# Kernel tuning notes

Hardware: AMD Instinct MI355X
Metric: run time of the kernel (lower is better)

Reference implementation:

```python
import jax, jax.numpy as jnp
from jax import lax
import numpy as np

D_IN, D_H, M_BANK = 1024, 512, 100


def setup_inputs() -> dict:
    key = jax.random.key(0)
    ks = jax.random.split(key, 12)
    B, T = 128, 256
    s = 0.01
    return {
        "hidden_frames": jax.random.normal(ks[0], (B, T, D_IN), jnp.float32),
        # hidden_to_content: Linear(hidden+input -> hidden)
        "W_c": jax.random.normal(ks[1], (D_H + D_IN, D_H), jnp.float32) * s,
        "b_c": jnp.zeros((D_H,), jnp.float32),
        # read_prob: Linear(hidden+input -> memory_bank_size)
        "W_rp": jax.random.normal(ks[2], (D_H + D_IN, M_BANK), jnp.float32) * s,
        "b_rp": jnp.zeros((M_BANK,), jnp.float32),
        # write_prob: Linear(hidden+input -> memory_bank_size)
        "W_wp": jax.random.normal(ks[3], (D_H + D_IN, M_BANK), jnp.float32) * s,
        "b_wp": jnp.zeros((M_BANK,), jnp.float32),
        # RNN cell params (init: normal(0, 0.01), bias zero)
        "Wxh": jax.random.normal(ks[4], (D_IN, D_H), jnp.float32) * s,
        "Wrh": jax.random.normal(ks[5], (D_H, D_H), jnp.float32) * s,
        "Whh": jax.random.normal(ks[6], (D_H, D_H), jnp.float32) * s,
        "bh": jnp.zeros((D_H,), jnp.float32),
        "nImg": 256,
    }


def reference(hidden_frames, W_c, b_c, W_rp, b_rp, W_wp, b_wp, Wxh, Wrh, Whh, bh, nImg):
    B = hidden_frames.shape[0]
    H = Wxh.shape[1]
    M = W_rp.shape[1]

    def step(carry, x_t):
        # x_t: (B, D_in); h: (B, H); mem: (B, M, H)
        h, mem = carry
        xh = jnp.concatenate([x_t, h], axis=-1)            # (B, D_in+H)
        ar = jax.nn.softmax(xh @ W_rp + b_rp, axis=-1)     # (B, M) read weights
        r = jnp.einsum('bm,bmh->bh', ar, mem)              # (B, H) read vector
        h_new = jax.nn.relu(x_t @ Wxh + r @ Wrh + h @ Whh + bh)
        c = jax.nn.relu(xh @ W_c + b_c)                    # (B, H) write content
        aw = jax.nn.softmax(xh @ W_wp + b_wp, axis=-1)[:, :, None]  # (B, M, 1)
        mem = aw * c[:, None, :] + (1.0 - aw) * mem        # gated blend overwrite
        return (h_new, mem), h_new

    xs = jnp.swapaxes(hidden_frames[:, :nImg, :], 0, 1)    # (T, B, D_in)
    h0 = jnp.zeros((B, H), hidden_frames.dtype)
    mem0 = jnp.zeros((B, M, H), hidden_frames.dtype)
    _, hs = lax.scan(step, (h0, mem0), xs)                 # hs: (T, B, H)
    return jnp.swapaxes(hs, 0, 1)                          # (B, T, H)
```

## Files before the change

kernel.cpp:

```cpp
#include <hip/hip_runtime.h>

#define D_IN   1024
#define D_H    512
#define M_BANK 100
#define BATCH  128
#define NCOL   1224
#define NPAD   1280
#define KTOT   1536
#define KSH    4

typedef unsigned short u16;
typedef __attribute__((ext_vector_type(8))) short s16x8;
typedef __attribute__((ext_vector_type(4))) float f32x4;

__device__ __forceinline__ u16 f2bf(float f) {
  union { float f; unsigned int u; } v;
  v.f = f;
  unsigned int r = (v.u + 0x7FFFu + ((v.u >> 16) & 1u)) >> 16;
  return (u16)r;
}
__device__ __forceinline__ float bf2f(u16 b) {
  union { unsigned int u; float f; } v;
  v.u = ((unsigned int)b) << 16;
  return v.f;
}

__global__ void k_prep_w(const float* __restrict__ W_c,
                         const float* __restrict__ W_rp,
                         const float* __restrict__ W_wp,
                         const float* __restrict__ Wxh,
                         const float* __restrict__ Whh,
                         u16* __restrict__ W_bt) {
  const int j = blockIdx.x;
  const int k = blockIdx.y * 256 + threadIdx.x;
  float v = 0.f;
  if (j < 100)       v = W_rp[(size_t)k * M_BANK + j];
  else if (j < 200)  v = W_wp[(size_t)k * M_BANK + (j - 100)];
  else if (j < 712)  v = W_c[(size_t)k * D_H + (j - 200)];
  else if (j < NCOL) v = (k < D_IN) ? Wxh[(size_t)k * D_H + (j - 712)]
                                    : Whh[(size_t)(k - D_IN) * D_H + (j - 712)];
  W_bt[(size_t)j * KTOT + k] = f2bf(v);
}

__global__ void k_prep_wrh(const float* __restrict__ Wrh,
                           u16* __restrict__ Wrh_bf) {
  const int i = blockIdx.x * 256 + threadIdx.x;
  Wrh_bf[i] = f2bf(Wrh[i]);
}

__global__ void k_zx_mfma(const float* __restrict__ frames,
                          const u16* __restrict__ W_bt,
                          float* __restrict__ zx,
                          int t0, int CH, int lgCH, int TF) {
  __shared__ u16 Asb[64][40];
  __shared__ u16 Bsb[64][40];
  const int tid  = threadIdx.x;
  const int lane = tid & 63;
  const int wid  = tid >> 6;
  const int wm   = wid >> 1, wn = wid & 1;
  const int j0 = blockIdx.x * 64;
  const int r0 = blockIdx.y * 64;
  const int srow = tid >> 2;
  const int skk  = (tid & 3) * 8;
  const int gr = r0 + srow;
  const int b  = gr >> lgCH;
  const int tc = gr & (CH - 1);
  const float* arow = &frames[((size_t)b * TF + t0 + tc) * D_IN];
  const u16*   brow = &W_bt[(size_t)(j0 + srow) * KTOT];

  f32x4 a00 = {0.f, 0.f, 0.f, 0.f}, a01 = {0.f, 0.f, 0.f, 0.f};
  f32x4 a10 = {0.f, 0.f, 0.f, 0.f}, a11 = {0.f, 0.f, 0.f, 0.f};

  for (int k0 = 0; k0 < D_IN; k0 += 32) {
    const float4 v0 = *reinterpret_cast<const float4*>(&arow[k0 + skk]);
    const float4 v1 = *reinterpret_cast<const float4*>(&arow[k0 + skk + 4]);
    s16x8 a8;
    a8[0] = (short)f2bf(v0.x); a8[1] = (short)f2bf(v0.y);
    a8[2] = (short)f2bf(v0.z); a8[3] = (short)f2bf(v0.w);
    a8[4] = (short)f2bf(v1.x); a8[5] = (short)f2bf(v1.y);
    a8[6] = (short)f2bf(v1.z); a8[7] = (short)f2bf(v1.w);
    *reinterpret_cast<s16x8*>(&Asb[srow][skk]) = a8;
    *reinterpret_cast<s16x8*>(&Bsb[srow][skk]) =
        *reinterpret_cast<const s16x8*>(&brow[k0 + skk]);
    __syncthreads();
    const int ka = (lane >> 4) * 8;
    const s16x8 af0 = *reinterpret_cast<s16x8*>(&Asb[wm * 32 + (lane & 15)][ka]);
    const s16x8 af1 = *reinterpret_cast<s16x8*>(&Asb[wm * 32 + 16 + (lane & 15)][ka]);
    const s16x8 bf0 = *reinterpret_cast<s16x8*>(&Bsb[wn * 32 + (lane & 15)][ka]);
    const s16x8 bf1 = *reinterpret_cast<s16x8*>(&Bsb[wn * 32 + 16 + (lane & 15)][ka]);
    a00 = __builtin_amdgcn_mfma_f32_16x16x32_bf16(af0, bf0, a00, 0, 0, 0);
    a01 = __builtin_amdgcn_mfma_f32_16x16x32_bf16(af0, bf1, a01, 0, 0, 0);
    a10 = __builtin_amdgcn_mfma_f32_16x16x32_bf16(af1, bf0, a10, 0, 0, 0);
    a11 = __builtin_amdgcn_mfma_f32_16x16x32_bf16(af1, bf1, a11, 0, 0, 0);
    __syncthreads();
  }
  const int rb = r0 + wm * 32 + (lane >> 4) * 4;
  const int cb = j0 + wn * 32 + (lane & 15);
#define STORE_ACC(A, MF, NF)                                             \
  {                                                                      \
    _Pragma("unroll")                                                    \
    for (int reg = 0; reg < 4; ++reg)                                    \
      zx[(size_t)(rb + MF * 16 + reg) * NPAD + cb + NF * 16] = A[reg];   \
  }
  STORE_ACC(a00, 0, 0) STORE_ACC(a01, 0, 1) STORE_ACC(a10, 1, 0) STORE_ACC(a11, 1, 1)
#undef STORE_ACC
}

__global__ void __launch_bounds__(256)
k_zh_mfma(const u16* __restrict__ h_bf,
          const u16* __restrict__ W_bt,
          float* __restrict__ zhp) {
  __shared__ u16 Asb[64][136];
  __shared__ u16 Bsb[64][136];
  const int tid  = threadIdx.x;
  const int lane = tid & 63;
  const int wid  = tid >> 6;
  const int wm   = wid >> 1, wn = wid & 1;
  const int j0 = blockIdx.x * 64;
  const int r0 = blockIdx.y * 64;
  const int kp = blockIdx.z;
  const int srow = tid >> 2;
  const int sseg = (tid & 3) * 32;
  const u16* arow = &h_bf[(size_t)(r0 + srow) * D_H + kp * 128 + sseg];
  const u16* brow = &W_bt[(size_t)(j0 + srow) * KTOT + D_IN + kp * 128 + sseg];

  #pragma unroll
  for (int i = 0; i < 4; ++i) {
    *reinterpret_cast<s16x8*>(&Asb[srow][sseg + i * 8]) =
        *reinterpret_cast<const s16x8*>(&arow[i * 8]);
    *reinterpret_cast<s16x8*>(&Bsb[srow][sseg + i * 8]) =
        *reinterpret_cast<const s16x8*>(&brow[i * 8]);
  }
  __syncthreads();

  f32x4 a00 = {0.f, 0.f, 0.f, 0.f}, a01 = {0.f, 0.f, 0.f, 0.f};
  f32x4 a10 = {0.f, 0.f, 0.f, 0.f}, a11 = {0.f, 0.f, 0.f, 0.f};
  const int la = lane & 15;
  #pragma unroll
  for (int kk = 0; kk < 4; ++kk) {
    const int ka = kk * 32 + (lane >> 4) * 8;
    const s16x8 af0 = *reinterpret_cast<s16x8*>(&Asb[wm * 32 + la][ka]);
    const s16x8 af1 = *reinterpret_cast<s16x8*>(&Asb[wm * 32 + 16 + la][ka]);
    const s16x8 bf0 = *reinterpret_cast<s16x8*>(&Bsb[wn * 32 + la][ka]);
    const s16x8 bf1 = *reinterpret_cast<s16x8*>(&Bsb[wn * 32 + 16 + la][ka]);
    a00 = __builtin_amdgcn_mfma_f32_16x16x32_bf16(af0, bf0, a00, 0, 0, 0);
    a01 = __builtin_amdgcn_mfma_f32_16x16x32_bf16(af0, bf1, a01, 0, 0, 0);
    a10 = __builtin_amdgcn_mfma_f32_16x16x32_bf16(af1, bf0, a10, 0, 0, 0);
    a11 = __builtin_amdgcn_mfma_f32_16x16x32_bf16(af1, bf1, a11, 0, 0, 0);
  }
  const int rb = r0 + wm * 32 + (lane >> 4) * 4;
  const int cb = j0 + wn * 32 + (lane & 15);
  float* zp = &zhp[(size_t)kp * BATCH * NPAD];
#define STORE_ACC(A, MF, NF)                                             \
  {                                                                      \
    _Pragma("unroll")                                                    \
    for (int reg = 0; reg < 4; ++reg)                                    \
      zp[(size_t)(rb + MF * 16 + reg) * NPAD + cb + NF * 16] = A[reg];   \
  }
  STORE_ACC(a00, 0, 0) STORE_ACC(a01, 0, 1) STORE_ACC(a10, 1, 0) STORE_ACC(a11, 1, 1)
#undef STORE_ACC
}

__global__ void __launch_bounds__(512)
k_phase2(const float* __restrict__ zx,
         const float* __restrict__ zhp,
         const u16* __restrict__ Wrh_bf,
         const float* __restrict__ b_rp,
         const float* __restrict__ b_wp,
         const float* __restrict__ b_c,
         const float* __restrict__ bh,
         u16* __restrict__ M2b,
         float* __restrict__ out,
         u16* __restrict__ h_bf,
         int t, int tc, int CH, int T) {
  __shared__ float ar_s[2][M_BANK];
  __shared__ float aw_s[2][M_BANK];
  __shared__ float c_s[2][D_H];
  __shared__ float red[2][16][32][4];
  __shared__ float smx[2][2][2];
  __shared__ float ssm[2][2][2];
  const int tid  = threadIdx.x;
  const int ba   = tid >> 8;
  const int lane = tid & 31;
  const int p    = blockIdx.x;
  const int b0   = blockIdx.y * 2;
  const int b_g  = b0 + ba;
  const int s0   = p * 128 + lane * 4;
  const bool hz  = (t > 0);
  const size_t zxrow = (size_t)(b_g * CH + tc) * NPAD;

  {
    const int u     = tid & 255;
    const int which = u >> 7;
    const int m     = u & 127;
    const int wv    = (u >> 6) & 1;
    float l = -1e30f;
    if (m < M_BANK) {
      const int col = which * 100 + m;
      l = (which ? b_wp[m] : b_rp[m]) + zx[zxrow + col];
      if (hz) {
        #pragma unroll
        for (int q = 0; q < KSH; ++q)
          l += zhp[(size_t)(q * BATCH + b_g) * NPAD + col];
      }
    }
    float mx = l;
    #pragma unroll
    for (int o = 32; o; o >>= 1) mx = fmaxf(mx, __shfl_xor(mx, o, 64));
    if ((tid & 63) == 0) smx[ba][which][wv] = mx;
    __syncthreads();
    mx = fmaxf(smx[ba][which][0], smx[ba][which][1]);
    const float e = (m < M_BANK) ? __expf(l - mx) : 0.f;
    float s = e;
    #pragma unroll
    for (int o = 32; o; o >>= 1) s += __shfl_xor(s, o, 64);
    if ((tid & 63) == 0) ssm[ba][which][wv] = s;
    __syncthreads();
    s = ssm[ba][which][0] + ssm[ba][which][1];
    if (m < M_BANK) {
      const float a = e / s;
      if (which) aw_s[ba][m] = a;
      else       ar_s[ba][m] = a;
    }
  }
  for (int idx = tid; idx < 2 * D_H; idx += 512) {
    const int bb  = idx >> 9;
    const int k   = idx & 511;
    const int bg2 = b0 + bb;
    float v = b_c[k] + zx[(size_t)(bg2 * CH + tc) * NPAD + 200 + k];
    if (hz) {
      #pragma unroll
      for (int q = 0; q < KSH; ++q)
        v += zhp[(size_t)(q * BATCH + bg2) * NPAD + 200 + k];
    }
    c_s[bb][k] = fmaxf(v, 0.f);
  }
  __syncthreads();

  {
    const int g = tid >> 5;
    float cwa[4] = {};
    float cwb[4] = {};
    const int kbase = g * 32;
    #pragma unroll 8
    for (int kk = 0; kk < 32; ++kk) {
      const int k = kbase + kk;
      const ushort4 w4 = *reinterpret_cast<const ushort4*>(&Wrh_bf[(size_t)k * D_H + s0]);
      const float w0 = bf2f(w4.x), w1 = bf2f(w4.y), w2 = bf2f(w4.z), w3 = bf2f(w4.w);
      const float ca = c_s[0][k];
      const float cb = c_s[1][k];
      cwa[0] += ca * w0; cwa[1] += ca * w1; cwa[2] += ca * w2; cwa[3] += ca * w3;
      cwb[0] += cb * w0; cwb[1] += cb * w1; cwb[2] += cb * w2; cwb[3] += cb * w3;
    }
    #pragma unroll
    for (int j = 0; j < 4; ++j) {
      red[0][g][lane][j] = cwa[j];
      red[1][g][lane][j] = cwb[j];
    }
  }
  __syncthreads();
  float cw[4] = {};
  #pragma unroll
  for (int gg = 0; gg < 16; ++gg)
    #pragma unroll
    for (int j = 0; j < 4; ++j) cw[j] += red[ba][gg][lane][j];
  __syncthreads();

  const int mg    = (tid >> 5) & 7;
  const int mcnt  = (mg < 4) ? 13 : 12;
  const int mbase = (mg < 4) ? mg * 13 : 52 + (mg - 4) * 12;
  float racc[4] = {};
  u16* mp = &M2b[((size_t)b_g * M_BANK + mbase) * D_H + s0];
  for (int mm = 0; mm < mcnt; ++mm) {
    const int m = mbase + mm;
    const ushort4 v4 = *reinterpret_cast<const ushort4*>(mp);
    const float v0 = bf2f(v4.x), v1 = bf2f(v4.y), v2 = bf2f(v4.z), v3 = bf2f(v4.w);
    const float a = ar_s[ba][m];
    const float w = aw_s[ba][m];
    racc[0] += a * v0; racc[1] += a * v1; racc[2] += a * v2; racc[3] += a * v3;
    ushort4 nv;
    nv.x = f2bf(w * cw[0] + (1.f - w) * v0);
    nv.y = f2bf(w * cw[1] + (1.f - w) * v1);
    nv.z = f2bf(w * cw[2] + (1.f - w) * v2);
    nv.w = f2bf(w * cw[3] + (1.f - w) * v3);
    *reinterpret_cast<ushort4*>(mp) = nv;
    mp += D_H;
  }
  #pragma unroll
  for (int j = 0; j < 4; ++j) red[ba][mg][lane][j] = racc[j];
  __syncthreads();

  if ((tid & 255) < 32) {
    float ph[4];
    const float4 vb = *reinterpret_cast<const float4*>(&bh[s0]);
    const float4 px = *reinterpret_cast<const float4*>(&zx[zxrow + 712 + s0]);
    ph[0] = vb.x + px.x; ph[1] = vb.y + px.y;
    ph[2] = vb.z + px.z; ph[3] = vb.w + px.w;
    #pragma unroll
    for (int gg = 0; gg < 8; ++gg)
      #pragma unroll
      for (int j = 0; j < 4; ++j) ph[j] += red[ba][gg][lane][j];
    if (hz) {
      #pragma unroll
      for (int q = 0; q < KSH; ++q) {
        const float4 pz = *reinterpret_cast<const float4*>(
            &zhp[(size_t)(q * BATCH + b_g) * NPAD + 712 + s0]);
        ph[0] += pz.x; ph[1] += pz.y; ph[2] += pz.z; ph[3] += pz.w;
      }
    }
    float4 h;
    h.x = fmaxf(ph[0], 0.f); h.y = fmaxf(ph[1], 0.f);
    h.z = fmaxf(ph[2], 0.f); h.w = fmaxf(ph[3], 0.f);
    *reinterpret_cast<float4*>(&out[((size_t)b_g * T + t) * D_H + s0]) = h;
    ushort4 hb;
    hb.x = f2bf(h.x); hb.y = f2bf(h.y); hb.z = f2bf(h.z); hb.w = f2bf(h.w);
    *reinterpret_cast<ushort4*>(&h_bf[(size_t)b_g * D_H + s0]) = hb;
  }
}

extern "C" void kernel_launch(void* const* d_in, const int* in_sizes, int n_in,
                              void* d_out, int out_size, void* d_ws, size_t ws_size,
                              hipStream_t stream) {
  const float* frames = (const float*)d_in[0];
  const float* W_c    = (const float*)d_in[1];
  const float* b_c    = (const float*)d_in[2];
  const float* W_rp   = (const float*)d_in[3];
  const float* b_rp   = (const float*)d_in[4];
  const float* W_wp   = (const float*)d_in[5];
  const float* b_wp   = (const float*)d_in[6];
  const float* Wxh    = (const float*)d_in[7];
  const float* Wrh    = (const float*)d_in[8];
  const float* Whh    = (const float*)d_in[9];
  const float* bh     = (const float*)d_in[10];
  float* out = (float*)d_out;

  const int TF = in_sizes[0] / (BATCH * D_IN);
  const int T  = out_size / (BATCH * D_H);

  const size_t M2B_FL   = (size_t)BATCH * M_BANK * D_H / 2;
  const size_t ZHP_FL   = (size_t)KSH * BATCH * NPAD;
  const size_t WBT_FL   = (size_t)NPAD * KTOT / 2;
  const size_t WRH_FL   = (size_t)D_H * D_H / 2;
  const size_t HBF_FL   = (size_t)BATCH * D_H / 2;

  u16*   M2b = (u16*)d_ws;
  float* zhp = (float*)d_ws + M2B_FL;
  float* zx  = zhp + ZHP_FL;

  int CH = 32, lgCH = 5;
  while (CH > 1 &&
         ((M2B_FL + ZHP_FL + WBT_FL + WRH_FL + HBF_FL +
           (size_t)BATCH * CH * NPAD) * sizeof(float) > ws_size ||
          (T % CH) != 0)) {
    CH >>= 1; --lgCH;
  }

  u16* W_bt   = (u16*)(zx + (size_t)BATCH * CH * NPAD);
  u16* Wrh_bf = W_bt + (size_t)NPAD * KTOT;
  u16* h_bf   = Wrh_bf + (size_t)D_H * D_H;

  hipMemsetAsync(M2b, 0, M2B_FL * sizeof(float), stream);
  k_prep_w<<<dim3(NPAD, KTOT / 256), 256, 0, stream>>>(W_c, W_rp, W_wp, Wxh, Whh, W_bt);
  k_prep_wrh<<<dim3(D_H * D_H / 256), 256, 0, stream>>>(Wrh, Wrh_bf);

  for (int t0 = 0; t0 < T; t0 += CH) {
    k_zx_mfma<<<dim3(NPAD / 64, BATCH * CH / 64), 256, 0, stream>>>(
        frames, W_bt, zx, t0, CH, lgCH, TF);
    for (int t = t0; t < t0 + CH; ++t) {
      if (t > 0)
        k_zh_mfma<<<dim3(NPAD / 64, BATCH / 64, KSH), 256, 0, stream>>>(h_bf, W_bt, zhp);
      k_phase2<<<dim3(D_H / 128, BATCH / 2), 512, 0, stream>>>(
          zx, zhp, Wrh_bf, b_rp, b_wp, b_c, bh, M2b, out, h_bf, t, t - t0, CH, T);
    }
  }
}
```

Baseline: 4.419 ms.

## Fuse per-step hidden GEMM and phase2 into one kernel with flag sync

Merges the per-timestep hidden-state GEMM kernel and the phase2 kernel into a single 256-block launch. The first 160 blocks compute zh partial products and signal completion through agent-scope atomic counters, and all blocks spin-wait on the counter for their batch half before the softmax and memory update. The hidden state is double-buffered so the GEMM reads h_r while phase2 writes h_w. This removes one kernel launch per timestep but relies on all 256 blocks being co-resident to avoid deadlock, and adds spin-wait latency.

```diff
diff --git a/kernel.cpp b/kernel.cpp
--- a/kernel.cpp
+++ b/kernel.cpp
@@ -8,6 +8,8 @@
 #define NPAD   1280
 #define KTOT   1536
 #define KSH    4
+#define NZH    160
+#define ZH_TGT 80
 
 typedef unsigned short u16;
 typedef __attribute__((ext_vector_type(8))) short s16x8;
@@ -106,88 +108,101 @@
 #undef STORE_ACC
 }
 
-__global__ void __launch_bounds__(256)
-k_zh_mfma(const u16* __restrict__ h_bf,
-          const u16* __restrict__ W_bt,
-          float* __restrict__ zhp) {
-  __shared__ u16 Asb[64][136];
-  __shared__ u16 Bsb[64][136];
+__global__ void __launch_bounds__(512)
+k_step2(const float* __restrict__ zx,
+        float* __restrict__ zhp,
+        const u16* __restrict__ W_bt,
+        const u16* __restrict__ Wrh_bf,
+        const float* __restrict__ b_rp,
+        const float* __restrict__ b_wp,
+        const float* __restrict__ b_c,
+        const float* __restrict__ bh,
+        u16* __restrict__ M2b,
+        float* __restrict__ out,
+        const u16* __restrict__ h_r,
+        u16* __restrict__ h_w,
+        int* __restrict__ flags,
+        int t, int tc, int CH, int T) {
+  __shared__ float smem[8704];
+  u16* Asb = (u16*)smem;
+  u16* Bsb = Asb + 64 * 136;
+  float* ar_s = smem;
+  float* aw_s = smem + 200;
+  float* c_s  = smem + 400;
+  float* red  = smem + 1424;
+  float* smx  = smem + 5520;
+  float* ssm  = smem + 5528;
+
   const int tid  = threadIdx.x;
-  const int lane = tid & 63;
-  const int wid  = tid >> 6;
-  const int wm   = wid >> 1, wn = wid & 1;
-  const int j0 = blockIdx.x * 64;
-  const int r0 = blockIdx.y * 64;
-  const int kp = blockIdx.z;
-  const int srow = tid >> 2;
-  const int sseg = (tid & 3) * 32;
-  const u16* arow = &h_bf[(size_t)(r0 + srow) * D_H + kp * 128 + sseg];
-  const u16* brow = &W_bt[(size_t)(j0 + srow) * KTOT + D_IN + kp * 128 + sseg];
-
-  #pragma unroll
-  for (int i = 0; i < 4; ++i) {
-    *reinterpret_cast<s16x8*>(&Asb[srow][sseg + i * 8]) =
-        *reinterpret_cast<const s16x8*>(&arow[i * 8]);
-    *reinterpret_cast<s16x8*>(&Bsb[srow][sseg + i * 8]) =
-        *reinterpret_cast<const s16x8*>(&brow[i * 8]);
-  }
-  __syncthreads();
-
-  f32x4 a00 = {0.f, 0.f, 0.f, 0.f}, a01 = {0.f, 0.f, 0.f, 0.f};
-  f32x4 a10 = {0.f, 0.f, 0.f, 0.f}, a11 = {0.f, 0.f, 0.f, 0.f};
-  const int la = lane & 15;
-  #pragma unroll
-  for (int kk = 0; kk < 4; ++kk) {
-    const int ka = kk * 32 + (lane >> 4) * 8;
-    const s16x8 af0 = *reinterpret_cast<s16x8*>(&Asb[wm * 32 + la][ka]);
-    const s16x8 af1 = *reinterpret_cast<s16x8*>(&Asb[wm * 32 + 16 + la][ka]);
-    const s16x8 bf0 = *reinterpret_cast<s16x8*>(&Bsb[wn * 32 + la][ka]);
-    const s16x8 bf1 = *reinterpret_cast<s16x8*>(&Bsb[wn * 32 + 16 + la][ka]);
-    a00 = __builtin_amdgcn_mfma_f32_16x16x32_bf16(af0, bf0, a00, 0, 0, 0);
-    a01 = __builtin_amdgcn_mfma_f32_16x16x32_bf16(af0, bf1, a01, 0, 0, 0);
-    a10 = __builtin_amdgcn_mfma_f32_16x16x32_bf16(af1, bf0, a10, 0, 0, 0);
-    a11 = __builtin_amdgcn_mfma_f32_16x16x32_bf16(af1, bf1, a11, 0, 0, 0);
-  }
-  const int rb = r0 + wm * 32 + (lane >> 4) * 4;
-  const int cb = j0 + wn * 32 + (lane & 15);
-  float* zp = &zhp[(size_t)kp * BATCH * NPAD];
-#define STORE_ACC(A, MF, NF)                                             \
-  {                                                                      \
-    _Pragma("unroll")                                                    \
-    for (int reg = 0; reg < 4; ++reg)                                    \
-      zp[(size_t)(rb + MF * 16 + reg) * NPAD + cb + NF * 16] = A[reg];   \
-  }
-  STORE_ACC(a00, 0, 0) STORE_ACC(a01, 0, 1) STORE_ACC(a10, 1, 0) STORE_ACC(a11, 1, 1)
-#undef STORE_ACC
-}
-
-__global__ void __launch_bounds__(512)
-k_phase2(const float* __restrict__ zx,
-         const float* __restrict__ zhp,
-         const u16* __restrict__ Wrh_bf,
-         const float* __restrict__ b_rp,
-         const float* __restrict__ b_wp,
-         const float* __restrict__ b_c,
-         const float* __restrict__ bh,
-         u16* __restrict__ M2b,
-         float* __restrict__ out,
-         u16* __restrict__ h_bf,
-         int t, int tc, int CH, int T) {
-  __shared__ float ar_s[2][M_BANK];
-  __shared__ float aw_s[2][M_BANK];
-  __shared__ float c_s[2][D_H];
-  __shared__ float red[2][16][32][4];
-  __shared__ float smx[2][2][2];
-  __shared__ float ssm[2][2][2];
-  const int tid  = threadIdx.x;
+  const int beta = blockIdx.x;
+
+  if (t > 0 && beta < NZH) {
+    const int jt = beta % 20;
+    const int w  = beta / 20;
+    const int bt = w & 1;
+    const int kp = w >> 1;
+    const int j0 = jt * 64, r0 = bt * 64;
+    const int srow = tid >> 3;
+    const int sseg = (tid & 7) * 16;
+    const u16* arow = &h_r[(size_t)(r0 + srow) * D_H + kp * 128 + sseg];
+    const u16* brow = &W_bt[(size_t)(j0 + srow) * KTOT + D_IN + kp * 128 + sseg];
+    *reinterpret_cast<s16x8*>(&Asb[srow * 136 + sseg]) =
+        *reinterpret_cast<const s16x8*>(&arow[0]);
+    *reinterpret_cast<s16x8*>(&Asb[srow * 136 + sseg + 8]) =
+        *reinterpret_cast<const s16x8*>(&arow[8]);
+    *reinterpret_cast<s16x8*>(&Bsb[srow * 136 + sseg]) =
+        *reinterpret_cast<const s16x8*>(&brow[0]);
+    *reinterpret_cast<s16x8*>(&Bsb[srow * 136 + sseg + 8]) =
+        *reinterpret_cast<const s16x8*>(&brow[8]);
+    __syncthreads();
+
+    const int lane = tid & 63;
+    const int wid  = tid >> 6;
+    const int wm   = wid >> 2;
+    const int wn   = wid & 3;
+    const int la   = lane & 15;
+    f32x4 a0 = {0.f, 0.f, 0.f, 0.f}, a1 = {0.f, 0.f, 0.f, 0.f};
+    #pragma unroll
+    for (int kk = 0; kk < 4; ++kk) {
+      const int ka = kk * 32 + (lane >> 4) * 8;
+      const s16x8 af0 = *reinterpret_cast<s16x8*>(&Asb[(wm * 32 + la) * 136 + ka]);
+      const s16x8 af1 = *reinterpret_cast<s16x8*>(&Asb[(wm * 32 + 16 + la) * 136 + ka]);
+      const s16x8 bf  = *reinterpret_cast<s16x8*>(&Bsb[(wn * 16 + la) * 136 + ka]);
+      a0 = __builtin_amdgcn_mfma_f32_16x16x32_bf16(af0, bf, a0, 0, 0, 0);
+      a1 = __builtin_amdgcn_mfma_f32_16x16x32_bf16(af1, bf, a1, 0, 0, 0);
+    }
+    float* zp = &zhp[(size_t)kp * BATCH * NPAD];
+    const int rb = r0 + wm * 32 + (lane >> 4) * 4;
+    const int cb = j0 + wn * 16 + la;
+    #pragma unroll
+    for (int reg = 0; reg < 4; ++reg) {
+      zp[(size_t)(rb + reg) * NPAD + cb]      = a0[reg];
+      zp[(size_t)(rb + 16 + reg) * NPAD + cb] = a1[reg];
+    }
+    __syncthreads();
+    if (tid == 0)
+      __hip_atomic_fetch_add(&flags[t * 2 + bt], 1,
+                             __ATOMIC_RELEASE, __HIP_MEMORY_SCOPE_AGENT);
+  }
+
   const int ba   = tid >> 8;
   const int lane = tid & 31;
-  const int p    = blockIdx.x;
-  const int b0   = blockIdx.y * 2;
+  const int p    = beta & 3;
+  const int by   = beta >> 2;
+  const int b0   = by * 2;
   const int b_g  = b0 + ba;
   const int s0   = p * 128 + lane * 4;
   const bool hz  = (t > 0);
   const size_t zxrow = (size_t)(b_g * CH + tc) * NPAD;
+
+  if (hz) {
+    if (tid == 0) {
+      while (__hip_atomic_load(&flags[t * 2 + (by >> 5)],
+                               __ATOMIC_ACQUIRE, __HIP_MEMORY_SCOPE_AGENT) < ZH_TGT)
+        __builtin_amdgcn_s_sleep(2);
+    }
+    __syncthreads();
+  }
 
   {
     const int u     = tid & 255;
@@ -207,20 +222,20 @@
     float mx = l;
     #pragma unroll
     for (int o = 32; o; o >>= 1) mx = fmaxf(mx, __shfl_xor(mx, o, 64));
-    if ((tid & 63) == 0) smx[ba][which][wv] = mx;
-    __syncthreads();
-    mx = fmaxf(smx[ba][which][0], smx[ba][which][1]);
+    if ((tid & 63) == 0) smx[ba * 4 + which * 2 + wv] = mx;
+    __syncthreads();
+    mx = fmaxf(smx[ba * 4 + which * 2], smx[ba * 4 + which * 2 + 1]);
     const float e = (m < M_BANK) ? __expf(l - mx) : 0.f;
     float s = e;
     #pragma unroll
     for (int o = 32; o; o >>= 1) s += __shfl_xor(s, o, 64);
-    if ((tid & 63) == 0) ssm[ba][which][wv] = s;
-    __syncthreads();
-    s = ssm[ba][which][0] + ssm[ba][which][1];
+    if ((tid & 63) == 0) ssm[ba * 4 + which * 2 + wv] = s;
+    __syncthreads();
+    s = ssm[ba * 4 + which * 2] + ssm[ba * 4 + which * 2 + 1];
     if (m < M_BANK) {
       const float a = e / s;
-      if (which) aw_s[ba][m] = a;
-      else       ar_s[ba][m] = a;
+      if (which) aw_s[ba * M_BANK + m] = a;
+      else       ar_s[ba * M_BANK + m] = a;
     }
   }
   for (int idx = tid; idx < 2 * D_H; idx += 512) {
@@ -233,7 +248,7 @@
       for (int q = 0; q < KSH; ++q)
         v += zhp[(size_t)(q * BATCH + bg2) * NPAD + 200 + k];
     }
-    c_s[bb][k] = fmaxf(v, 0.f);
+    c_s[bb * D_H + k] = fmaxf(v, 0.f);
   }
   __syncthreads();
 
@@ -247,15 +262,15 @@
       const int k = kbase + kk;
       const ushort4 w4 = *reinterpret_cast<const ushort4*>(&Wrh_bf[(size_t)k * D_H + s0]);
       const float w0 = bf2f(w4.x), w1 = bf2f(w4.y), w2 = bf2f(w4.z), w3 = bf2f(w4.w);
-      const float ca = c_s[0][k];
-      const float cb = c_s[1][k];
+      const float ca = c_s[k];
+      const float cb = c_s[D_H + k];
       cwa[0] += ca * w0; cwa[1] += ca * w1; cwa[2] += ca * w2; cwa[3] += ca * w3;
       cwb[0] += cb * w0; cwb[1] += cb * w1; cwb[2] += cb * w2; cwb[3] += cb * w3;
     }
     #pragma unroll
     for (int j = 0; j < 4; ++j) {
-      red[0][g][lane][j] = cwa[j];
-      red[1][g][lane][j] = cwb[j];
+      red[((0 * 16 + g) * 32 + lane) * 4 + j] = cwa[j];
+      red[((1 * 16 + g) * 32 + lane) * 4 + j] = cwb[j];
     }
   }
   __syncthreads();
@@ -263,7 +278,7 @@
   #pragma unroll
   for (int gg = 0; gg < 16; ++gg)
     #pragma unroll
-    for (int j = 0; j < 4; ++j) cw[j] += red[ba][gg][lane][j];
+    for (int j = 0; j < 4; ++j) cw[j] += red[((ba * 16 + gg) * 32 + lane) * 4 + j];
   __syncthreads();
 
   const int mg    = (tid >> 5) & 7;
@@ -275,8 +290,8 @@
     const int m = mbase + mm;
     const ushort4 v4 = *reinterpret_cast<const ushort4*>(mp);
     const float v0 = bf2f(v4.x), v1 = bf2f(v4.y), v2 = bf2f(v4.z), v3 = bf2f(v4.w);
-    const float a = ar_s[ba][m];
-    const float w = aw_s[ba][m];
+    const float a = ar_s[ba * M_BANK + m];
+    const float w = aw_s[ba * M_BANK + m];
     racc[0] += a * v0; racc[1] += a * v1; racc[2] += a * v2; racc[3] += a * v3;
     ushort4 nv;
     nv.x = f2bf(w * cw[0] + (1.f - w) * v0);
@@ -287,7 +302,7 @@
     mp += D_H;
   }
   #pragma unroll
-  for (int j = 0; j < 4; ++j) red[ba][mg][lane][j] = racc[j];
+  for (int j = 0; j < 4; ++j) red[((ba * 16 + mg) * 32 + lane) * 4 + j] = racc[j];
   __syncthreads();
 
   if ((tid & 255) < 32) {
@@ -299,7 +314,7 @@
     #pragma unroll
     for (int gg = 0; gg < 8; ++gg)
       #pragma unroll
-      for (int j = 0; j < 4; ++j) ph[j] += red[ba][gg][lane][j];
+      for (int j = 0; j < 4; ++j) ph[j] += red[((ba * 16 + gg) * 32 + lane) * 4 + j];
     if (hz) {
       #pragma unroll
       for (int q = 0; q < KSH; ++q) {
@@ -314,7 +329,7 @@
     *reinterpret_cast<float4*>(&out[((size_t)b_g * T + t) * D_H + s0]) = h;
     ushort4 hb;
     hb.x = f2bf(h.x); hb.y = f2bf(h.y); hb.z = f2bf(h.z); hb.w = f2bf(h.w);
-    *reinterpret_cast<ushort4*>(&h_bf[(size_t)b_g * D_H + s0]) = hb;
+    *reinterpret_cast<ushort4*>(&h_w[(size_t)b_g * D_H + s0]) = hb;
   }
 }
 
@@ -337,11 +352,12 @@
   const int TF = in_sizes[0] / (BATCH * D_IN);
   const int T  = out_size / (BATCH * D_H);
 
-  const size_t M2B_FL   = (size_t)BATCH * M_BANK * D_H / 2;
-  const size_t ZHP_FL   = (size_t)KSH * BATCH * NPAD;
-  const size_t WBT_FL   = (size_t)NPAD * KTOT / 2;
-  const size_t WRH_FL   = (size_t)D_H * D_H / 2;
-  const size_t HBF_FL   = (size_t)BATCH * D_H / 2;
+  const size_t M2B_FL = (size_t)BATCH * M_BANK * D_H / 2;
+  const size_t ZHP_FL = (size_t)KSH * BATCH * NPAD;
+  const size_t WBT_FL = (size_t)NPAD * KTOT / 2;
+  const size_t WRH_FL = (size_t)D_H * D_H / 2;
+  const size_t HBF_FL = (size_t)BATCH * D_H;
+  const size_t FLG_FL = 2048;
 
   u16*   M2b = (u16*)d_ws;
   float* zhp = (float*)d_ws + M2B_FL;
@@ -349,7 +365,7 @@
 
   int CH = 32, lgCH = 5;
   while (CH > 1 &&
-         ((M2B_FL + ZHP_FL + WBT_FL + WRH_FL + HBF_FL +
+         ((M2B_FL + ZHP_FL + WBT_FL + WRH_FL + HBF_FL + FLG_FL +
            (size_t)BATCH * CH * NPAD) * sizeof(float) > ws_size ||
           (T % CH) != 0)) {
     CH >>= 1; --lgCH;
@@ -357,9 +373,13 @@
 
   u16* W_bt   = (u16*)(zx + (size_t)BATCH * CH * NPAD);
   u16* Wrh_bf = W_bt + (size_t)NPAD * KTOT;
-  u16* h_bf   = Wrh_bf + (size_t)D_H * D_H;
+  u16* hbuf0  = Wrh_bf + (size_t)D_H * D_H;
+  u16* hbuf1  = hbuf0 + (size_t)BATCH * D_H;
+  int* flags  = (int*)(hbuf1 + (size_t)BATCH * D_H);
+  u16* hb[2]  = {hbuf0, hbuf1};
 
   hipMemsetAsync(M2b, 0, M2B_FL * sizeof(float), stream);
+  hipMemsetAsync(flags, 0, (size_t)2 * T * sizeof(int), stream);
   k_prep_w<<<dim3(NPAD, KTOT / 256), 256, 0, stream>>>(W_c, W_rp, W_wp, Wxh, Whh, W_bt);
   k_prep_wrh<<<dim3(D_H * D_H / 256), 256, 0, stream>>>(Wrh, Wrh_bf);
 
@@ -367,10 +387,9 @@
     k_zx_mfma<<<dim3(NPAD / 64, BATCH * CH / 64), 256, 0, stream>>>(
         frames, W_bt, zx, t0, CH, lgCH, TF);
     for (int t = t0; t < t0 + CH; ++t) {
-      if (t > 0)
-        k_zh_mfma<<<dim3(NPAD / 64, BATCH / 64, KSH), 256, 0, stream>>>(h_bf, W_bt, zhp);
-      k_phase2<<<dim3(D_H / 128, BATCH / 2), 512, 0, stream>>>(
-          zx, zhp, Wrh_bf, b_rp, b_wp, b_c, bh, M2b, out, h_bf, t, t - t0, CH, T);
-    }
-  }
-}
+      k_step2<<<256, 512, 0, stream>>>(
+          zx, zhp, W_bt, Wrh_bf, b_rp, b_wp, b_c, bh, M2b, out,
+          hb[t & 1], hb[(t + 1) & 1], flags, t, t - t0, CH, T);
+    }
+  }
+}
```

New measurement: 9.135 ms. 2.07x slower.
